# Kernel tuning notes

Measured on AMD Instinct MI355X. Metric: run time of the kernel, lower is better.

Reference implementation:

```python
import jax, jax.numpy as jnp
import numpy as np

NUM_EMBED = 1024
NUM_HEADS = 16
NUM_LAYER = 8
BLOCK_SIZE = 1024
VOCAB = 32000
B, T = 4, 1024
HEAD_SIZE = NUM_EMBED // NUM_HEADS


def _ln(x, g, b, eps=1e-5):
    mu = jnp.mean(x, axis=-1, keepdims=True)
    var = jnp.var(x, axis=-1, keepdims=True)
    return (x - mu) * jax.lax.rsqrt(var + eps) * g + b


def setup_inputs() -> dict:
    key = jax.random.key(0)
    ks = jax.random.split(key, 16)
    C, L, V = NUM_EMBED, NUM_LAYER, VOCAB
    std = 0.02
    n = lambda k, shp: jax.random.normal(k, shp, jnp.float32) * std
    return {
        "x": jax.random.randint(ks[0], (B, T), 0, V),
        "tok_emb": n(ks[1], (V, C)),
        "pos_emb": n(ks[2], (BLOCK_SIZE, C)),
        "Wq": n(ks[3], (L, C, C)),
        "Wk": n(ks[4], (L, C, C)),
        "Wv": n(ks[5], (L, C, C)),
        "Wproj": n(ks[6], (L, C, C)),
        "bproj": jnp.zeros((L, C), jnp.float32),
        "ln1_g": jnp.ones((L, C), jnp.float32),
        "ln1_b": jnp.zeros((L, C), jnp.float32),
        "ln2_g": jnp.ones((L, C), jnp.float32),
        "ln2_b": jnp.zeros((L, C), jnp.float32),
        "W1": n(ks[7], (L, C, 4 * C)),
        "b1": jnp.zeros((L, 4 * C), jnp.float32),
        "W2": n(ks[8], (L, 4 * C, C)),
        "b2": jnp.zeros((L, C), jnp.float32),
        "lnf_g": jnp.ones((C,), jnp.float32),
        "lnf_b": jnp.zeros((C,), jnp.float32),
        "Whead": n(ks[9], (C, V)),
    }


def _forward(x, tok_emb, pos_emb, Wq, Wk, Wv, Wproj, bproj,
             ln1_g, ln1_b, ln2_g, ln2_b, W1, b1, W2, b2,
             lnf_g, lnf_b, Whead):
    Bc, Tc = x.shape
    H, hs = NUM_HEADS, HEAD_SIZE
    h = tok_emb[x] + pos_emb[:Tc]  # [B,T,C]
    causal = jnp.tril(jnp.ones((Tc, Tc), bool))
    neg_inf = jnp.finfo(h.dtype).min
    for l in range(NUM_LAYER):
        xn = _ln(h, ln1_g[l], ln1_b[l])
        q = (xn @ Wq[l]).reshape(Bc, Tc, H, hs)
        k = (xn @ Wk[l]).reshape(Bc, Tc, H, hs)
        v = (xn @ Wv[l]).reshape(Bc, Tc, H, hs)
        att = jnp.einsum('bqhd,bkhd->bhqk', q, k) * (hs ** -0.5)
        att = jnp.where(causal, att, neg_inf)
        att = jax.nn.softmax(att, axis=-1)  # dropout p=0 in eval
        o = jnp.einsum('bhqk,bkhd->bqhd', att, v).reshape(Bc, Tc, H * hs)
        h = h + o @ Wproj[l] + bproj[l]
        xn = _ln(h, ln2_g[l], ln2_b[l])
        h = h + jax.nn.relu(xn @ W1[l] + b1[l]) @ W2[l] + b2[l]
    h = _ln(h, lnf_g, lnf_b)
    return h @ Whead  # logits [B,T,V]


def reference(x, tok_emb, pos_emb, Wq, Wk, Wv, Wproj, bproj,
              ln1_g, ln1_b, ln2_g, ln2_b, W1, b1, W2, b2,
              lnf_g, lnf_b, Whead):
    return _forward(x, tok_emb, pos_emb, Wq, Wk, Wv, Wproj, bproj,
                    ln1_g, ln1_b, ln2_g, ln2_b, W1, b1, W2, b2,
                    lnf_g, lnf_b, Whead)
```

## Files before the change

kernel.cpp:

```cpp
#include <hip/hip_runtime.h>
#include <stdint.h>
#include <stddef.h>

#define C_DIM 1024
#define T_DIM 1024
#define B_DIM 4
#define L_DIM 8
#define V_DIM 32000
#define HS 64
#define NHEAD 16
#define NROWS (B_DIM * T_DIM)
#define LDQ   3072

typedef __bf16 bf16_t;
typedef __attribute__((ext_vector_type(8))) __bf16 bf16x8;
typedef __attribute__((ext_vector_type(4))) __bf16 bf16x4;
typedef __attribute__((ext_vector_type(4))) float f32x4;
typedef unsigned int u32;
typedef unsigned short u16;

static __device__ __forceinline__ f32x4 mfma16(bf16x8 a, bf16x8 b, f32x4 c) {
    return __builtin_amdgcn_mfma_f32_16x16x32_bf16(a, b, c, 0, 0, 0);
}

static __device__ __forceinline__ void gl_lds16(const bf16_t* g, bf16_t* l) {
    __builtin_amdgcn_global_load_lds(
        (const __attribute__((address_space(1))) u32*)(const void*)g,
        (__attribute__((address_space(3))) u32*)(void*)l, 16, 0, 0);
}

__global__ __launch_bounds__(256) void embed_kernel(
    const int* __restrict__ x, const float* __restrict__ tok,
    const float* __restrict__ pos, float* __restrict__ h) {
    int idx = blockIdx.x * 256 + threadIdx.x;
    int row = idx >> 8;
    int c4  = (idx & 255) * 4;
    int t   = row & (T_DIM - 1);
    int tk  = x[row];
    float4 a = *(const float4*)(tok + (size_t)tk * C_DIM + c4);
    float4 p = *(const float4*)(pos + (size_t)t * C_DIM + c4);
    float4 r;
    r.x = a.x + p.x; r.y = a.y + p.y; r.z = a.z + p.z; r.w = a.w + p.w;
    *(float4*)(h + (size_t)row * C_DIM + c4) = r;
}

static __device__ __forceinline__ void wtr_tile(
    const float* __restrict__ in, bf16_t* __restrict__ out,
    int K, int N, int n0, int k0, int tid) {
    __shared__ float t[64][65];
    int tx = tid & 63, tw = tid >> 6;
#pragma unroll 4
    for (int i = 0; i < 16; ++i) {
        int k = tw * 16 + i;
        t[k][tx] = in[(size_t)(k0 + k) * N + n0 + tx];
    }
    __syncthreads();
#pragma unroll 4
    for (int i = 0; i < 16; ++i) {
        int n = tw * 16 + i;
        out[(size_t)(n0 + n) * K + k0 + tx] = (bf16_t)t[tx][n];
    }
}

__global__ __launch_bounds__(256) void wtr_kernel(
    const float* __restrict__ in, bf16_t* __restrict__ out, int K, int N) {
    wtr_tile(in, out, K, N, blockIdx.x * 64, blockIdx.y * 64, threadIdx.x);
}

__global__ __launch_bounds__(256) void wtr_layer_kernel(
    const float* __restrict__ Wq, const float* __restrict__ Wk,
    const float* __restrict__ Wv, const float* __restrict__ Wp,
    const float* __restrict__ W1, const float* __restrict__ W2,
    bf16_t* __restrict__ qkvT, bf16_t* __restrict__ projT,
    bf16_t* __restrict__ w1T, bf16_t* __restrict__ w2T) {
    int b = blockIdx.x;
    const float* in; bf16_t* out; int K, N, tn, tk;
    if (b < 1024) {
        int which = b >> 8, t = b & 255;
        in  = which == 0 ? Wq : which == 1 ? Wk : which == 2 ? Wv : Wp;
        out = which < 3 ? qkvT + (size_t)which * C_DIM * C_DIM : projT;
        K = C_DIM; N = C_DIM; tn = t & 15; tk = t >> 4;
    } else if (b < 2048) {
        int t = b - 1024; in = W1; out = w1T;
        K = C_DIM; N = 4 * C_DIM; tn = t & 63; tk = t >> 6;
    } else {
        int t = b - 2048; in = W2; out = w2T;
        K = 4 * C_DIM; N = C_DIM; tn = t & 15; tk = t >> 4;
    }
    wtr_tile(in, out, K, N, tn * 64, tk * 64, threadIdx.x);
}

__global__ __launch_bounds__(256) void ln_kernel(
    const float* __restrict__ x, const float* __restrict__ gam,
    const float* __restrict__ bet, bf16_t* __restrict__ out) {
    int wave = threadIdx.x >> 6, lane = threadIdx.x & 63;
    int row  = blockIdx.x * 4 + wave;
    const float* xr = x + (size_t)row * C_DIM;
    float4 v[4];
    float s = 0.f, sq = 0.f;
#pragma unroll
    for (int i = 0; i < 4; ++i) {
        v[i] = *(const float4*)(xr + i * 256 + lane * 4);
        s  += v[i].x + v[i].y + v[i].z + v[i].w;
        sq += v[i].x * v[i].x + v[i].y * v[i].y + v[i].z * v[i].z + v[i].w * v[i].w;
    }
#pragma unroll
    for (int m = 1; m < 64; m <<= 1) {
        s  += __shfl_xor(s, m);
        sq += __shfl_xor(sq, m);
    }
    float mu  = s * (1.f / 1024.f);
    float var = sq * (1.f / 1024.f) - mu * mu;
    float rs  = rsqrtf(var + 1e-5f);
    bf16_t* orow = out + (size_t)row * C_DIM;
#pragma unroll
    for (int i = 0; i < 4; ++i) {
        int c = i * 256 + lane * 4;
        float4 g4 = *(const float4*)(gam + c);
        float4 b4 = *(const float4*)(bet + c);
        bf16x4 o;
        o[0] = (bf16_t)((v[i].x - mu) * rs * g4.x + b4.x);
        o[1] = (bf16_t)((v[i].y - mu) * rs * g4.y + b4.y);
        o[2] = (bf16_t)((v[i].z - mu) * rs * g4.z + b4.z);
        o[3] = (bf16_t)((v[i].w - mu) * rs * g4.w + b4.w);
        *(bf16x4*)(orow + c) = o;
    }
}

template <int MODE>
__global__ __launch_bounds__(256) void gemm_kernel(
    const bf16_t* __restrict__ A, const bf16_t* __restrict__ Bt,
    const float* __restrict__ bias, void* __restrict__ Cout,
    int M, int N, int K) {
    __shared__ bf16_t Asm[2][128 * 32];
    __shared__ bf16_t Bsm[2][128 * 32];

    const int tid  = threadIdx.x;
    const int nwg  = gridDim.x;
    int bid = blockIdx.x;
    if ((nwg & 7) == 0) {
        int cpx = nwg >> 3;
        bid = (bid & 7) * cpx + (bid >> 3);
    }
    const int MT = M >> 7;
    const int mt = bid % MT, nt = bid / MT;
    const int mbase = mt << 7, nbase = nt << 7;
    const int wave = tid >> 6, lane = tid & 63;
    const int lr = lane & 15, lg = lane >> 4;
    const int wm = wave >> 1, wn = wave & 1;
    const int NK = K >> 5;

    const int srow = lane >> 2;
    const int ssw  = (((lane & 3) ^ ((lane >> 3) & 3)) << 3);
    const bf16_t* aRow = A  + (size_t)(mbase + wave * 32 + srow) * K + ssw;
    const bf16_t* bRow = Bt + (size_t)(nbase + wave * 32 + srow) * K + ssw;
    const int ldsW = wave * 1024;

#define STAGE(buf, kt)                                                        \
    do {                                                                      \
        const bf16_t* ag = aRow + (size_t)(kt) * 32;                          \
        const bf16_t* bg = bRow + (size_t)(kt) * 32;                          \
        gl_lds16(ag,            &Asm[buf][ldsW]);                             \
        gl_lds16(ag + 16 * K,   &Asm[buf][ldsW + 512]);                       \
        gl_lds16(bg,            &Bsm[buf][ldsW]);                             \
        gl_lds16(bg + 16 * K,   &Bsm[buf][ldsW + 512]);                       \
    } while (0)

    STAGE(0, 0);
    __syncthreads();

    f32x4 acc[4][4] = {};
    const int rsw = ((lg ^ ((lr >> 1) & 3)) << 3);
    int buf = 0;
    for (int kt = 0; kt < NK; ++kt) {
        if (kt + 1 < NK) STAGE(buf ^ 1, kt + 1);
        bf16x8 af[4], bfr[4];
#pragma unroll
        for (int i = 0; i < 4; ++i)
            af[i] = *(const bf16x8*)&Asm[buf][(wm * 64 + i * 16 + lr) * 32 + rsw];
#pragma unroll
        for (int j = 0; j < 4; ++j)
            bfr[j] = *(const bf16x8*)&Bsm[buf][(wn * 64 + j * 16 + lr) * 32 + rsw];
#pragma unroll
        for (int i = 0; i < 4; ++i)
#pragma unroll
            for (int j = 0; j < 4; ++j)
                acc[i][j] = mfma16(af[i], bfr[j], acc[i][j]);
        __syncthreads();
        buf ^= 1;
    }
#undef STAGE

    float bj[4];
#pragma unroll
    for (int j = 0; j < 4; ++j)
        bj[j] = bias ? bias[nbase + wn * 64 + j * 16 + lr] : 0.0f;
#pragma unroll
    for (int i = 0; i < 4; ++i) {
#pragma unroll
        for (int j = 0; j < 4; ++j) {
            int col = nbase + wn * 64 + j * 16 + lr;
#pragma unroll
            for (int e = 0; e < 4; ++e) {
                int row = mbase + wm * 64 + i * 16 + lg * 4 + e;
                float val = acc[i][j][e] + bj[j];
                size_t off = (size_t)row * N + col;
                if (MODE == 0) {
                    ((bf16_t*)Cout)[off] = (bf16_t)val;
                } else if (MODE == 1) {
                    ((bf16_t*)Cout)[off] = (bf16_t)fmaxf(val, 0.0f);
                } else if (MODE == 2) {
                    ((float*)Cout)[off] += val;
                } else {
                    ((float*)Cout)[off] = val;
                }
            }
        }
    }
}

__global__ __launch_bounds__(256) void attn_kernel(
    const bf16_t* __restrict__ Qb, const bf16_t* __restrict__ Kb,
    const bf16_t* __restrict__ Vb, bf16_t* __restrict__ Ob) {
    __shared__ bf16_t Ksm[2][64][72];
    __shared__ bf16_t Vsm[2][64][72];
    __shared__ bf16_t Psm[4][32][72];

    const int tid  = threadIdx.x;
    const int bid  = blockIdx.x;
    const int qt   = bid & 7;
    const int hh   = (bid >> 3) & 15;
    const int bb   = bid >> 7;
    const int wave = tid >> 6, lane = tid & 63;
    const int lr = lane & 15, lg = lane >> 4;
    const int qbase = qt * 128 + wave * 32;
    const size_t basei = ((size_t)bb * T_DIM) * LDQ + hh * HS;
    const size_t baseo = ((size_t)bb * T_DIM) * C_DIM + hh * HS;

    bf16x8 qf[2][2];
#pragma unroll
    for (int rb = 0; rb < 2; ++rb) {
        const bf16_t* qrow = Qb + basei + (size_t)(qbase + rb * 16 + lr) * LDQ;
        qf[rb][0] = *(const bf16x8*)(qrow + lg * 8);
        qf[rb][1] = *(const bf16x8*)(qrow + 32 + lg * 8);
    }

    f32x4 o[2][4] = {};
    float m_run[2][4], l_run[2][4];
#pragma unroll
    for (int rb = 0; rb < 2; ++rb)
#pragma unroll
        for (int e = 0; e < 4; ++e) { m_run[rb][e] = -1e30f; l_run[rb][e] = 0.f; }

    const int krow = tid >> 2, kc = (tid & 3) * 8;
    const bf16_t* kgp = Kb + basei + (size_t)krow * LDQ + kc;
    const int vds = (tid & 7) * 8, vkg = (tid >> 3) * 2;
    const bf16_t* vgp0 = Vb + basei + (size_t)vkg * LDQ + vds;
    const bf16_t* vgp1 = vgp0 + LDQ;

    const int nkt = 2 * qt + 2;

    uint4 k0r, k1r, v0r, v1r;
    k0r = *(const uint4*)(kgp);
    k1r = *(const uint4*)(kgp + 32);
    v0r = *(const uint4*)(vgp0);
    v1r = *(const uint4*)(vgp1);
    *(uint4*)&Ksm[0][krow][kc]      = k0r;
    *(uint4*)&Ksm[0][krow][kc + 32] = k1r;
    {
        const u16* e0 = (const u16*)&v0r;
        const u16* e1 = (const u16*)&v1r;
#pragma unroll
        for (int j = 0; j < 8; ++j)
            *(u32*)&Vsm[0][vds + j][vkg] = (u32)e0[j] | ((u32)e1[j] << 16);
    }
    __syncthreads();

    for (int kt = 0; kt < nkt; ++kt) {
        const int c = kt & 1;
        if (kt + 1 < nkt) {
            const size_t go = (size_t)(kt + 1) * 64 * LDQ;
            k0r = *(const uint4*)(kgp + go);
            k1r = *(const uint4*)(kgp + go + 32);
            v0r = *(const uint4*)(vgp0 + go);
            v1r = *(const uint4*)(vgp1 + go);
        }

        f32x4 s[2][4];
#pragma unroll
        for (int kk = 0; kk < 4; ++kk) {
            bf16x8 kf0 = *(const bf16x8*)&Ksm[c][kk * 16 + lr][lg * 8];
            bf16x8 kf1 = *(const bf16x8*)&Ksm[c][kk * 16 + lr][32 + lg * 8];
#pragma unroll
            for (int rb = 0; rb < 2; ++rb) {
                f32x4 z = {};
                z = mfma16(qf[rb][0], kf0, z);
                z = mfma16(qf[rb][1], kf1, z);
                s[rb][kk] = z;
            }
        }
        if (kt * 64 + 63 > qbase) {
#pragma unroll
            for (int rb = 0; rb < 2; ++rb)
#pragma unroll
                for (int kk = 0; kk < 4; ++kk)
#pragma unroll
                    for (int e = 0; e < 4; ++e) {
                        int key = kt * 64 + kk * 16 + lr;
                        int qi  = qbase + rb * 16 + lg * 4 + e;
                        float v = s[rb][kk][e] * 0.125f;
                        s[rb][kk][e] = (key <= qi) ? v : -1e30f;
                    }
        } else {
#pragma unroll
            for (int rb = 0; rb < 2; ++rb)
#pragma unroll
                for (int kk = 0; kk < 4; ++kk)
#pragma unroll
                    for (int e = 0; e < 4; ++e)
                        s[rb][kk][e] *= 0.125f;
        }

#pragma unroll
        for (int rb = 0; rb < 2; ++rb) {
#pragma unroll
            for (int e = 0; e < 4; ++e) {
                float v = fmaxf(fmaxf(s[rb][0][e], s[rb][1][e]),
                                fmaxf(s[rb][2][e], s[rb][3][e]));
                v = fmaxf(v, __shfl_xor(v, 1));
                v = fmaxf(v, __shfl_xor(v, 2));
                v = fmaxf(v, __shfl_xor(v, 4));
                v = fmaxf(v, __shfl_xor(v, 8));
                float mn    = fmaxf(m_run[rb][e], v);
                float alpha = __expf(m_run[rb][e] - mn);
                m_run[rb][e] = mn;
                float ssum = 0.f;
#pragma unroll
                for (int kk = 0; kk < 4; ++kk) {
                    float p = __expf(s[rb][kk][e] - mn);
                    Psm[wave][rb * 16 + lg * 4 + e][kk * 16 + lr] = (bf16_t)p;
                    ssum += p;
                }
                ssum += __shfl_xor(ssum, 1);
                ssum += __shfl_xor(ssum, 2);
                ssum += __shfl_xor(ssum, 4);
                ssum += __shfl_xor(ssum, 8);
                l_run[rb][e] = l_run[rb][e] * alpha + ssum;
#pragma unroll
                for (int db = 0; db < 4; ++db)
                    o[rb][db][e] *= alpha;
            }
        }

        asm volatile("s_waitcnt lgkmcnt(0)" ::: "memory");
        bf16x8 pf[2][2];
#pragma unroll
        for (int rb = 0; rb < 2; ++rb)
#pragma unroll
            for (int h2 = 0; h2 < 2; ++h2)
                pf[rb][h2] = *(const bf16x8*)&Psm[wave][rb * 16 + lr][h2 * 32 + lg * 8];
#pragma unroll
        for (int h2 = 0; h2 < 2; ++h2)
#pragma unroll
            for (int db = 0; db < 4; ++db) {
                bf16x8 vf = *(const bf16x8*)&Vsm[c][db * 16 + lr][h2 * 32 + lg * 8];
#pragma unroll
                for (int rb = 0; rb < 2; ++rb)
                    o[rb][db] = mfma16(pf[rb][h2], vf, o[rb][db]);
            }

        if (kt + 1 < nkt) {
            const int w = c ^ 1;
            *(uint4*)&Ksm[w][krow][kc]      = k0r;
            *(uint4*)&Ksm[w][krow][kc + 32] = k1r;
            const u16* e0 = (const u16*)&v0r;
            const u16* e1 = (const u16*)&v1r;
#pragma unroll
            for (int j = 0; j < 8; ++j)
                *(u32*)&Vsm[w][vds + j][vkg] = (u32)e0[j] | ((u32)e1[j] << 16);
        }
        __syncthreads();
    }

#pragma unroll
    for (int rb = 0; rb < 2; ++rb)
#pragma unroll
        for (int e = 0; e < 4; ++e) {
            float inv = 1.0f / l_run[rb][e];
            bf16_t* orow = Ob + baseo + (size_t)(qbase + rb * 16 + lg * 4 + e) * C_DIM;
#pragma unroll
            for (int db = 0; db < 4; ++db)
                orow[db * 16 + lr] = (bf16_t)(o[rb][db][e] * inv);
        }
}

extern "C" void kernel_launch(void* const* d_in, const int* in_sizes, int n_in,
                              void* d_out, int out_size, void* d_ws, size_t ws_size,
                              hipStream_t stream) {
    const int*   x      = (const int*)d_in[0];
    const float* tok    = (const float*)d_in[1];
    const float* pos    = (const float*)d_in[2];
    const float* Wq     = (const float*)d_in[3];
    const float* Wk     = (const float*)d_in[4];
    const float* Wv     = (const float*)d_in[5];
    const float* Wproj  = (const float*)d_in[6];
    const float* bproj  = (const float*)d_in[7];
    const float* ln1_g  = (const float*)d_in[8];
    const float* ln1_b  = (const float*)d_in[9];
    const float* ln2_g  = (const float*)d_in[10];
    const float* ln2_b  = (const float*)d_in[11];
    const float* W1     = (const float*)d_in[12];
    const float* b1     = (const float*)d_in[13];
    const float* W2     = (const float*)d_in[14];
    const float* b2     = (const float*)d_in[15];
    const float* lnf_g  = (const float*)d_in[16];
    const float* lnf_b  = (const float*)d_in[17];
    const float* Whead  = (const float*)d_in[18];
    float* out = (float*)d_out;

    char* ws = (char*)d_ws;
    float*  h    = (float*)ws;   ws += (size_t)NROWS * C_DIM * 4;
    bf16_t* xn   = (bf16_t*)ws;  ws += (size_t)NROWS * C_DIM * 2;
    bf16_t* qkvb = (bf16_t*)ws;  ws += (size_t)NROWS * LDQ * 2;
    bf16_t* ob   = (bf16_t*)ws;  ws += (size_t)NROWS * C_DIM * 2;
    bf16_t* mid  = (bf16_t*)ws;  ws += (size_t)NROWS * 4 * C_DIM * 2;
    bf16_t* wT   = (bf16_t*)ws;  ws += (size_t)V_DIM * C_DIM * 2;

    const size_t M1 = (size_t)C_DIM * C_DIM;
    bf16_t* qkvT  = wT;
    bf16_t* projT = wT + 3 * M1;
    bf16_t* w1T   = wT + 4 * M1;
    bf16_t* w2T   = wT + 8 * M1;

    dim3 blk(256);

    embed_kernel<<<dim3(NROWS * C_DIM / 1024), blk, 0, stream>>>(x, tok, pos, h);

    for (int l = 0; l < L_DIM; ++l) {
        const size_t wo  = (size_t)l * M1;
        const size_t wo1 = (size_t)l * 4 * M1;

        wtr_layer_kernel<<<dim3(3072), blk, 0, stream>>>(
            Wq + wo, Wk + wo, Wv + wo, Wproj + wo, W1 + wo1, W2 + wo1,
            qkvT, projT, w1T, w2T);

        ln_kernel<<<dim3(NROWS / 4), blk, 0, stream>>>(h, ln1_g + l * C_DIM, ln1_b + l * C_DIM, xn);

        gemm_kernel<0><<<dim3(32 * 24), blk, 0, stream>>>(xn, qkvT, nullptr, qkvb, NROWS, LDQ, C_DIM);

        attn_kernel<<<dim3(B_DIM * NHEAD * (T_DIM / 128)), blk, 0, stream>>>(
            qkvb, qkvb + C_DIM, qkvb + 2 * C_DIM, ob);

        gemm_kernel<2><<<dim3(32 * 8), blk, 0, stream>>>(ob, projT, bproj + l * C_DIM, h, NROWS, C_DIM, C_DIM);

        ln_kernel<<<dim3(NROWS / 4), blk, 0, stream>>>(h, ln2_g + l * C_DIM, ln2_b + l * C_DIM, xn);

        gemm_kernel<1><<<dim3(32 * 32), blk, 0, stream>>>(xn, w1T, b1 + (size_t)l * 4 * C_DIM, mid, NROWS, 4 * C_DIM, C_DIM);
        gemm_kernel<2><<<dim3(32 * 8), blk, 0, stream>>>(mid, w2T, b2 + l * C_DIM, h, NROWS, C_DIM, 4 * C_DIM);
    }

    ln_kernel<<<dim3(NROWS / 4), blk, 0, stream>>>(h, lnf_g, lnf_b, xn);
    wtr_kernel<<<dim3(500, 16), blk, 0, stream>>>(Whead, wT, C_DIM, V_DIM);
    gemm_kernel<3><<<dim3(32 * 250), blk, 0, stream>>>(xn, wT, nullptr, out, NROWS, V_DIM, C_DIM);
}
```

Before: 2.827 ms.

## Batch all weight transposes, triple-buffer GEMM LDS, raise MFMA priority

Three separate changes. When the workspace is large enough, all layer weights and the head weight are transposed to bf16 in a single up-front launch instead of nine separate launches. The GEMM moves from a double-buffered to a triple-buffered LDS pipeline, using explicit vmcnt waits and a single barrier per k-step in place of two syncthreads. s_setprio is raised around the MFMA blocks in both the GEMM and attention kernels. The costs are more workspace, more LDS per block (which may lower occupancy), and a code path that depends on the workspace size.

```diff
diff --git a/kernel.cpp b/kernel.cpp
--- a/kernel.cpp
+++ b/kernel.cpp
@@ -90,6 +90,41 @@
     wtr_tile(in, out, K, N, tn * 64, tk * 64, threadIdx.x);
 }
 
+__global__ __launch_bounds__(256) void wtr_all_kernel(
+    const float* __restrict__ Wq, const float* __restrict__ Wk,
+    const float* __restrict__ Wv, const float* __restrict__ Wp,
+    const float* __restrict__ W1, const float* __restrict__ W2,
+    const float* __restrict__ Wh,
+    bf16_t* __restrict__ wAll, bf16_t* __restrict__ headT) {
+    const size_t M1 = (size_t)C_DIM * C_DIM;
+    int b = blockIdx.x;
+    if (b < 24576) {
+        int l = b / 3072, r = b % 3072;
+        const size_t wo  = (size_t)l * M1;
+        const size_t wo1 = (size_t)l * 4 * M1;
+        bf16_t* lw = wAll + (size_t)l * 12 * M1;
+        const float* in; bf16_t* out; int K, N, tn, tk;
+        if (r < 1024) {
+            int which = r >> 8, t = r & 255;
+            in  = (which == 0 ? Wq + wo : which == 1 ? Wk + wo :
+                   which == 2 ? Wv + wo : Wp + wo);
+            out = which < 3 ? lw + (size_t)which * M1 : lw + 3 * M1;
+            K = C_DIM; N = C_DIM; tn = t & 15; tk = t >> 4;
+        } else if (r < 2048) {
+            int t = r - 1024; in = W1 + wo1; out = lw + 4 * M1;
+            K = C_DIM; N = 4 * C_DIM; tn = t & 63; tk = t >> 6;
+        } else {
+            int t = r - 2048; in = W2 + wo1; out = lw + 8 * M1;
+            K = 4 * C_DIM; N = C_DIM; tn = t & 15; tk = t >> 4;
+        }
+        wtr_tile(in, out, K, N, tn * 64, tk * 64, threadIdx.x);
+    } else {
+        int b2 = b - 24576;
+        int tn = b2 % 500, tk = b2 / 500;
+        wtr_tile(Wh, headT, C_DIM, V_DIM, tn * 64, tk * 64, threadIdx.x);
+    }
+}
+
 __global__ __launch_bounds__(256) void ln_kernel(
     const float* __restrict__ x, const float* __restrict__ gam,
     const float* __restrict__ bet, bf16_t* __restrict__ out) {
@@ -132,8 +167,8 @@
     const bf16_t* __restrict__ A, const bf16_t* __restrict__ Bt,
     const float* __restrict__ bias, void* __restrict__ Cout,
     int M, int N, int K) {
-    __shared__ bf16_t Asm[2][128 * 32];
-    __shared__ bf16_t Bsm[2][128 * 32];
+    __shared__ bf16_t Asm[3][128 * 32];
+    __shared__ bf16_t Bsm[3][128 * 32];
 
     const int tid  = threadIdx.x;
     const int nwg  = gridDim.x;
@@ -167,27 +202,32 @@
     } while (0)
 
     STAGE(0, 0);
-    __syncthreads();
+    if (NK > 1) STAGE(1, 1);
 
     f32x4 acc[4][4] = {};
     const int rsw = ((lg ^ ((lr >> 1) & 3)) << 3);
-    int buf = 0;
     for (int kt = 0; kt < NK; ++kt) {
-        if (kt + 1 < NK) STAGE(buf ^ 1, kt + 1);
+        const int cur = kt % 3;
+        if (kt + 1 < NK) asm volatile("s_waitcnt vmcnt(4)" ::: "memory");
+        else             asm volatile("s_waitcnt vmcnt(0)" ::: "memory");
+        __builtin_amdgcn_s_barrier();
+        asm volatile("" ::: "memory");
+        __builtin_amdgcn_sched_barrier(0);
+        if (kt + 2 < NK) STAGE((kt + 2) % 3, kt + 2);
         bf16x8 af[4], bfr[4];
 #pragma unroll
         for (int i = 0; i < 4; ++i)
-            af[i] = *(const bf16x8*)&Asm[buf][(wm * 64 + i * 16 + lr) * 32 + rsw];
+            af[i] = *(const bf16x8*)&Asm[cur][(wm * 64 + i * 16 + lr) * 32 + rsw];
 #pragma unroll
         for (int j = 0; j < 4; ++j)
-            bfr[j] = *(const bf16x8*)&Bsm[buf][(wn * 64 + j * 16 + lr) * 32 + rsw];
+            bfr[j] = *(const bf16x8*)&Bsm[cur][(wn * 64 + j * 16 + lr) * 32 + rsw];
+        __builtin_amdgcn_s_setprio(1);
 #pragma unroll
         for (int i = 0; i < 4; ++i)
 #pragma unroll
             for (int j = 0; j < 4; ++j)
                 acc[i][j] = mfma16(af[i], bfr[j], acc[i][j]);
-        __syncthreads();
-        buf ^= 1;
+        __builtin_amdgcn_s_setprio(0);
     }
 #undef STAGE
 
@@ -287,6 +327,7 @@
         }
 
         f32x4 s[2][4];
+        __builtin_amdgcn_s_setprio(1);
 #pragma unroll
         for (int kk = 0; kk < 4; ++kk) {
             bf16x8 kf0 = *(const bf16x8*)&Ksm[c][kk * 16 + lr][lg * 8];
@@ -299,6 +340,7 @@
                 s[rb][kk] = z;
             }
         }
+        __builtin_amdgcn_s_setprio(0);
         if (kt * 64 + 63 > qbase) {
 #pragma unroll
             for (int rb = 0; rb < 2; ++rb)
@@ -359,6 +401,7 @@
 #pragma unroll
             for (int h2 = 0; h2 < 2; ++h2)
                 pf[rb][h2] = *(const bf16x8*)&Psm[wave][rb * 16 + lr][h2 * 32 + lg * 8];
+        __builtin_amdgcn_s_setprio(1);
 #pragma unroll
         for (int h2 = 0; h2 < 2; ++h2)
 #pragma unroll
@@ -368,6 +411,7 @@
                 for (int rb = 0; rb < 2; ++rb)
                     o[rb][db] = mfma16(pf[rb][h2], vf, o[rb][db]);
             }
+        __builtin_amdgcn_s_setprio(0);
 
         if (kt + 1 < nkt) {
             const int w = c ^ 1;
@@ -418,31 +462,47 @@
     const float* Whead  = (const float*)d_in[18];
     float* out = (float*)d_out;
 
+    const size_t M1 = (size_t)C_DIM * C_DIM;
     char* ws = (char*)d_ws;
     float*  h    = (float*)ws;   ws += (size_t)NROWS * C_DIM * 4;
     bf16_t* xn   = (bf16_t*)ws;  ws += (size_t)NROWS * C_DIM * 2;
     bf16_t* qkvb = (bf16_t*)ws;  ws += (size_t)NROWS * LDQ * 2;
     bf16_t* ob   = (bf16_t*)ws;  ws += (size_t)NROWS * C_DIM * 2;
     bf16_t* mid  = (bf16_t*)ws;  ws += (size_t)NROWS * 4 * C_DIM * 2;
-    bf16_t* wT   = (bf16_t*)ws;  ws += (size_t)V_DIM * C_DIM * 2;
-
-    const size_t M1 = (size_t)C_DIM * C_DIM;
-    bf16_t* qkvT  = wT;
-    bf16_t* projT = wT + 3 * M1;
-    bf16_t* w1T   = wT + 4 * M1;
-    bf16_t* w2T   = wT + 8 * M1;
+
+    const size_t used_act = (size_t)(ws - (char*)d_ws);
+    const size_t need_big = used_act + (8 * 12 * M1 + (size_t)V_DIM * C_DIM) * 2;
+    const bool big = ws_size >= need_big;
+
+    bf16_t* wAll = nullptr; bf16_t* headT = nullptr; bf16_t* wT = nullptr;
+    if (big) {
+        wAll  = (bf16_t*)ws;  ws += 8 * 12 * M1 * 2;
+        headT = (bf16_t*)ws;  ws += (size_t)V_DIM * C_DIM * 2;
+    } else {
+        wT    = (bf16_t*)ws;  ws += (size_t)V_DIM * C_DIM * 2;
+    }
 
     dim3 blk(256);
 
     embed_kernel<<<dim3(NROWS * C_DIM / 1024), blk, 0, stream>>>(x, tok, pos, h);
+    if (big)
+        wtr_all_kernel<<<dim3(24576 + 8000), blk, 0, stream>>>(
+            Wq, Wk, Wv, Wproj, W1, W2, Whead, wAll, headT);
 
     for (int l = 0; l < L_DIM; ++l) {
         const size_t wo  = (size_t)l * M1;
         const size_t wo1 = (size_t)l * 4 * M1;
 
-        wtr_layer_kernel<<<dim3(3072), blk, 0, stream>>>(
-            Wq + wo, Wk + wo, Wv + wo, Wproj + wo, W1 + wo1, W2 + wo1,
-            qkvT, projT, w1T, w2T);
+        bf16_t *qkvT, *projT, *w1T, *w2T;
+        if (big) {
+            bf16_t* lw = wAll + (size_t)l * 12 * M1;
+            qkvT = lw; projT = lw + 3 * M1; w1T = lw + 4 * M1; w2T = lw + 8 * M1;
+        } else {
+            qkvT = wT; projT = wT + 3 * M1; w1T = wT + 4 * M1; w2T = wT + 8 * M1;
+            wtr_layer_kernel<<<dim3(3072), blk, 0, stream>>>(
+                Wq + wo, Wk + wo, Wv + wo, Wproj + wo, W1 + wo1, W2 + wo1,
+                qkvT, projT, w1T, w2T);
+        }
 
         ln_kernel<<<dim3(NROWS / 4), blk, 0, stream>>>(h, ln1_g + l * C_DIM, ln1_b + l * C_DIM, xn);
 
@@ -460,6 +520,9 @@
     }
 
     ln_kernel<<<dim3(NROWS / 4), blk, 0, stream>>>(h, lnf_g, lnf_b, xn);
-    wtr_kernel<<<dim3(500, 16), blk, 0, stream>>>(Whead, wT, C_DIM, V_DIM);
-    gemm_kernel<3><<<dim3(32 * 250), blk, 0, stream>>>(xn, wT, nullptr, out, NROWS, V_DIM, C_DIM);
-}
+    if (!big) {
+        wtr_kernel<<<dim3(500, 16), blk, 0, stream>>>(Whead, wT, C_DIM, V_DIM);
+        headT = wT;
+    }
+    gemm_kernel<3><<<dim3(32 * 250), blk, 0, stream>>>(xn, headT, nullptr, out, NROWS, V_DIM, C_DIM);
+}
```

After: 3.323 ms. +17.6%, slower.
